# Optimization experiments

Hardware: AMD Instinct MI355X
Metric: run time of the kernel (lower is better)

The kernel has to match this reference:

```python
import jax, jax.numpy as jnp
import numpy as np

N = 32768          # total nodes
B = 64             # graphs
NPG = N // B       # nodes per graph (equal-sized graphs)
E = 524288         # edges (before self-loops)
D_IN, HID, HEADS, D_OUT = 128, 64, 4, 128
DH = HID * HEADS   # 256
NEG_SLOPE = 0.2
EPS = 1e-5

def _leaky(x):
    return jnp.where(x >= 0, x, NEG_SLOPE * x)

def gat_conv(x, src, dst, W, a_src, a_dst, b, concat):
    """PyG-style GATConv (self-loops already included in src/dst)."""
    H, C = a_src.shape
    h = (x @ W).reshape(N, H, C)                       # [N,H,C]
    es = jnp.einsum('nhc,hc->nh', h, a_src)            # score from source feats
    ed = jnp.einsum('nhc,hc->nh', h, a_dst)            # score from target feats
    e = _leaky(es[src] + ed[dst])                      # [E',H]
    m = jax.ops.segment_max(e, dst, num_segments=N)    # stable softmax per dst
    p = jnp.exp(e - m[dst])
    s = jax.ops.segment_sum(p, dst, num_segments=N)
    alpha = p / s[dst]                                 # [E',H]
    out = jax.ops.segment_sum(h[src] * alpha[..., None], dst, num_segments=N)
    out = out.reshape(N, H * C) if concat else out.mean(axis=1)
    return out + b

def mha(x, Wi, bi, Wo, bo, heads):
    """torch.nn.MultiheadAttention (batch_first, no mask, eval)."""
    Bb, T, D = x.shape
    qkv = x @ Wi.T + bi                                # [B,T,3D]
    q, k, v = jnp.split(qkv, 3, axis=-1)
    hd = D // heads
    def sp(t):
        return t.reshape(Bb, T, heads, hd).transpose(0, 2, 1, 3)  # [B,h,T,hd]
    q, k, v = sp(q), sp(k), sp(v)
    scores = jnp.einsum('bhqd,bhkd->bhqk', q, k) / jnp.sqrt(jnp.float32(hd))
    attn = jax.nn.softmax(scores, axis=-1)
    o = jnp.einsum('bhqk,bhkd->bhqd', attn, v)
    o = o.transpose(0, 2, 1, 3).reshape(Bb, T, D)
    return o @ Wo.T + bo

def layer_norm(x, g, b):
    mu = x.mean(-1, keepdims=True)
    var = x.var(-1, keepdims=True)
    return (x - mu) / jnp.sqrt(var + EPS) * g + b

def setup_inputs() -> dict:
    key = jax.random.key(0)
    ks = jax.random.split(key, 20)
    s = 0.1
    inp = {
        'x': jax.random.normal(ks[0], (N, D_IN), jnp.float32),
        'edge_index': jax.random.randint(ks[1], (2, E), 0, N, jnp.int64),
        'batch': (jnp.arange(N, dtype=jnp.int64) // NPG),
        # gat1: D_IN -> HEADS*HID (concat)
        'W1': jax.random.normal(ks[2], (D_IN, HEADS * HID), jnp.float32) * s,
        'aS1': jax.random.normal(ks[3], (HEADS, HID), jnp.float32) * s,
        'aD1': jax.random.normal(ks[4], (HEADS, HID), jnp.float32) * s,
        'b1': jnp.zeros((HEADS * HID,), jnp.float32),
        # gat2: DH -> HEADS*HID (concat)
        'W2': jax.random.normal(ks[5], (DH, HEADS * HID), jnp.float32) * s,
        'aS2': jax.random.normal(ks[6], (HEADS, HID), jnp.float32) * s,
        'aD2': jax.random.normal(ks[7], (HEADS, HID), jnp.float32) * s,
        'b2': jnp.zeros((HEADS * HID,), jnp.float32),
        # gat3: DH -> D_OUT, heads=1, concat=False (mean)
        'W3': jax.random.normal(ks[8], (DH, D_OUT), jnp.float32) * s,
        'aS3': jax.random.normal(ks[9], (1, D_OUT), jnp.float32) * s,
        'aD3': jax.random.normal(ks[10], (1, D_OUT), jnp.float32) * s,
        'b3': jnp.zeros((D_OUT,), jnp.float32),
        # MultiheadAttention
        'Wi': jax.random.normal(ks[11], (3 * DH, DH), jnp.float32) * s,
        'bi': jnp.zeros((3 * DH,), jnp.float32),
        'Wo': jax.random.normal(ks[12], (DH, DH), jnp.float32) * s,
        'bo': jnp.zeros((DH,), jnp.float32),
        # LayerNorm
        'gamma': jnp.ones((DH,), jnp.float32),
        'beta': jnp.zeros((DH,), jnp.float32),
    }
    return inp

def reference(x, edge_index, batch, W1, aS1, aD1, b1, W2, aS2, aD2, b2,
              W3, aS3, aD3, b3, Wi, bi, Wo, bo, gamma, beta):
    # add self-loops (PyG GATConv default)
    loops = jnp.arange(N, dtype=edge_index.dtype)
    src = jnp.concatenate([edge_index[0], loops])
    dst = jnp.concatenate([edge_index[1], loops])

    x1 = jax.nn.elu(gat_conv(x, src, dst, W1, aS1, aD1, b1, concat=True))
    x2 = jax.nn.elu(gat_conv(x1, src, dst, W2, aS2, aD2, b2, concat=True))

    # ragged-to-dense batching: batch = arange(N)//NPG (equal-sized, sorted),
    # so the torch python loop reduces to a reshape with no padding.
    x2b = x2.reshape(B, NPG, DH)
    attended = mha(x2b, Wi, bi, Wo, bo, HEADS).reshape(N, DH)

    x2a = layer_norm(attended + x2, gamma, beta)
    x3 = gat_conv(x2a, src, dst, W3, aS3, aD3, b3, concat=False)
    return x3
```

## Files before the change

kernel.cpp:

```cpp
#include <hip/hip_runtime.h>

typedef _Float16 half_t;
typedef _Float16 half8  __attribute__((ext_vector_type(8)));
typedef _Float16 half4v __attribute__((ext_vector_type(4)));
typedef float    f32x4  __attribute__((ext_vector_type(4)));

constexpr int N_NODES = 32768;
constexpr int NPG_    = 512;

#define MFMA16(a, b, c) __builtin_amdgcn_mfma_f32_16x16x32_f16((a), (b), (c), 0, 0, 0)

__device__ __forceinline__ void gload_lds16(const half_t* g, half_t* l) {
  __builtin_amdgcn_global_load_lds(
      (const __attribute__((address_space(1))) void*)g,
      (__attribute__((address_space(3))) void*)l, 16, 0, 0);
}

__global__ void k_hist(const int* __restrict__ dst, int* __restrict__ deg, int E) {
  int i = blockIdx.x * 256 + threadIdx.x;
  if (i < E) atomicAdd(&deg[dst[i]], 1);
}

__global__ __launch_bounds__(1024) void k_scan(const int* __restrict__ deg,
                                               int* __restrict__ rowptr) {
  __shared__ int part[1024];
  int t = threadIdx.x;
  int base = t * 32;
  int s = 0;
  #pragma unroll
  for (int i = 0; i < 32; i++) s += deg[base + i];
  part[t] = s;
  __syncthreads();
  for (int off = 1; off < 1024; off <<= 1) {
    int add = (t >= off) ? part[t - off] : 0;
    __syncthreads();
    part[t] += add;
    __syncthreads();
  }
  int run = (t == 0) ? 0 : part[t - 1];
  for (int i = 0; i < 32; i++) { rowptr[base + i] = run; run += deg[base + i]; }
  if (t == 1023) rowptr[N_NODES] = run;
}

__global__ void k_selfloop(const int* __restrict__ rowptr, int* __restrict__ fill,
                           int* __restrict__ col) {
  int i = blockIdx.x * 256 + threadIdx.x;
  fill[i] = 1;
  col[rowptr[i]] = i;
}

__global__ void k_scatter(const int* __restrict__ src, const int* __restrict__ dst,
                          const int* __restrict__ rowptr, int* __restrict__ fill,
                          int* __restrict__ col, int E) {
  int i = blockIdx.x * 256 + threadIdx.x;
  if (i < E) {
    int d = dst[i];
    int pos = rowptr[d] + atomicAdd(&fill[d], 1);
    col[pos] = src[i];
  }
}

__global__ void k_convert(
    const float* __restrict__ x,  half_t* __restrict__ x_h,
    const float* __restrict__ W1, half_t* __restrict__ W1t,
    const float* __restrict__ W2, half_t* __restrict__ W2t,
    const float* __restrict__ W3, half_t* __restrict__ W3t,
    const float* __restrict__ Wi, half_t* __restrict__ Wi_h,
    const float* __restrict__ Wo, half_t* __restrict__ Wo_h,
    int* __restrict__ deg)
{
  int bid = blockIdx.x, t = threadIdx.x;
  if (bid < 16384) {
    int i = bid * 256 + t;
    x_h[i] = (half_t)x[i];
  } else if (bid < 16512) {
    int i = (bid - 16384) * 256 + t;
    int o = i >> 7, k = i & 127;
    W1t[i] = (half_t)W1[k * 256 + o];
  } else if (bid < 16768) {
    int i = (bid - 16512) * 256 + t;
    int o = i >> 8, k = i & 255;
    W2t[i] = (half_t)W2[k * 256 + o];
  } else if (bid < 16896) {
    int i = (bid - 16768) * 256 + t;
    int o = i >> 8, k = i & 255;
    W3t[i] = (half_t)W3[k * 128 + o];
  } else if (bid < 17664) {
    int i = (bid - 16896) * 256 + t;
    Wi_h[i] = (half_t)Wi[i];
  } else if (bid < 17920) {
    int i = (bid - 17664) * 256 + t;
    Wo_h[i] = (half_t)Wo[i];
  } else {
    deg[(bid - 17920) * 256 + t] = 1;
  }
}

__global__ __launch_bounds__(256) void k_gemm(
    const half_t* __restrict__ A, const half_t* __restrict__ Bt,
    const float* __restrict__ bias, int bias_per_row,
    half_t* __restrict__ outh, float* __restrict__ outf,
    int M, int Nc, int K,
    const float* __restrict__ aS, const float* __restrict__ aD,
    float* __restrict__ es, float* __restrict__ ed, int H)
{
  __shared__ __align__(16) half_t As[128 * 64];
  __shared__ __align__(16) half_t Bs[128 * 64];
  __shared__ float sRed[2][4][64];
  int w = threadIdx.x >> 6, lane = threadIdx.x & 63;
  int r = lane & 15, q = lane >> 4;
  int m0 = blockIdx.y * 128, n0 = blockIdx.x * 128;
  int mh = (w & 1) * 64, nh = (w >> 1) * 64;
  f32x4 acc[4][4];
  #pragma unroll
  for (int i = 0; i < 4; i++)
    #pragma unroll
    for (int j = 0; j < 4; j++) acc[i][j] = f32x4{0.f, 0.f, 0.f, 0.f};

  int srow = lane >> 3;
  int sc   = lane & 7;

  for (int k0 = 0; k0 < K; k0 += 64) {
    __syncthreads();
    #pragma unroll
    for (int i = 0; i < 4; i++) {
      int R0 = w * 32 + i * 8;
      int row = R0 + srow;
      int cg = sc ^ (row & 7);
      gload_lds16(A  + (size_t)(m0 + row) * K + k0 + cg * 8, &As[R0 * 64]);
      gload_lds16(Bt + (size_t)(n0 + row) * K + k0 + cg * 8, &Bs[R0 * 64]);
    }
    __syncthreads();
    #pragma unroll
    for (int kk = 0; kk < 2; kk++) {
      half8 af[4], bf[4];
      #pragma unroll
      for (int t = 0; t < 4; t++) {
        int rr = mh + t * 16 + r;
        af[t] = *(const half8*)&As[rr * 64 + (((kk * 4 + q) ^ (rr & 7)) << 3)];
      }
      #pragma unroll
      for (int t = 0; t < 4; t++) {
        int rr = nh + t * 16 + r;
        bf[t] = *(const half8*)&Bs[rr * 64 + (((kk * 4 + q) ^ (rr & 7)) << 3)];
      }
      #pragma unroll
      for (int ti = 0; ti < 4; ti++)
        #pragma unroll
        for (int tj = 0; tj < 4; tj++)
          acc[ti][tj] = MFMA16(af[ti], bf[tj], acc[ti][tj]);
    }
  }

  #pragma unroll
  for (int tj = 0; tj < 4; tj++) {
    int colc = n0 + nh + tj * 16 + r;
    #pragma unroll
    for (int ti = 0; ti < 4; ti++) {
      #pragma unroll
      for (int i = 0; i < 4; i++) {
        int row = m0 + mh + ti * 16 + q * 4 + i;
        float bv = bias ? (bias_per_row ? bias[row] : bias[colc]) : 0.f;
        float v = acc[ti][tj][i] + bv;
        size_t idx = (size_t)row * Nc + colc;
        if (outf) outf[idx] = v;
        if (outh) outh[idx] = (half_t)v;
      }
    }
  }

  if (es) {
    if (H == 4) {
      int head = (n0 >> 6) + (nh >> 6);
      float aSv[4], aDv[4];
      #pragma unroll
      for (int tj = 0; tj < 4; tj++) {
        int cl = tj * 16 + r;
        aSv[tj] = aS[head * 64 + cl];
        aDv[tj] = aD[head * 64 + cl];
      }
      #pragma unroll
      for (int ti = 0; ti < 4; ti++) {
        #pragma unroll
        for (int i = 0; i < 4; i++) {
          float ps = 0.f, pd = 0.f;
          #pragma unroll
          for (int tj = 0; tj < 4; tj++) {
            float av = acc[ti][tj][i];
            ps += av * aSv[tj];
            pd += av * aDv[tj];
          }
          #pragma unroll
          for (int off = 1; off < 16; off <<= 1) {
            ps += __shfl_xor(ps, off);
            pd += __shfl_xor(pd, off);
          }
          if (r == 0) {
            int row = m0 + mh + ti * 16 + q * 4 + i;
            es[(size_t)row * 4 + head] = ps;
            ed[(size_t)row * 4 + head] = pd;
          }
        }
      }
    } else {
      float aSv[4], aDv[4];
      #pragma unroll
      for (int tj = 0; tj < 4; tj++) {
        int c = nh + tj * 16 + r;
        aSv[tj] = aS[c];
        aDv[tj] = aD[c];
      }
      #pragma unroll
      for (int ti = 0; ti < 4; ti++) {
        #pragma unroll
        for (int i = 0; i < 4; i++) {
          float ps = 0.f, pd = 0.f;
          #pragma unroll
          for (int tj = 0; tj < 4; tj++) {
            float av = acc[ti][tj][i];
            ps += av * aSv[tj];
            pd += av * aDv[tj];
          }
          #pragma unroll
          for (int off = 1; off < 16; off <<= 1) {
            ps += __shfl_xor(ps, off);
            pd += __shfl_xor(pd, off);
          }
          if (r == 0) {
            int ri = ti * 16 + q * 4 + i;
            sRed[0][w][ri] = ps;
            sRed[1][w][ri] = pd;
          }
        }
      }
      __syncthreads();
      if (threadIdx.x < 128) {
        int row = threadIdx.x;
        int wlo = row >> 6, ri = row & 63;
        es[m0 + row] = sRed[0][wlo][ri] + sRed[0][wlo + 2][ri];
        ed[m0 + row] = sRed[1][wlo][ri] + sRed[1][wlo + 2][ri];
      }
    }
  }
}

__global__ __launch_bounds__(256) void k_gemm_ln(
    const half_t* __restrict__ A, const half_t* __restrict__ Bt,
    const float* __restrict__ bias, const half_t* __restrict__ res,
    const float* __restrict__ gamma, const float* __restrict__ beta,
    half_t* __restrict__ outh)
{
  __shared__ __align__(16) half_t As[64 * 64];
  __shared__ __align__(16) half_t Bs[256 * 64];
  __shared__ float sSum[4][64], sSq[4][64];
  __shared__ float sMR[64][2];
  int w = threadIdx.x >> 6, lane = threadIdx.x & 63;
  int r = lane & 15, q = lane >> 4;
  int m0 = blockIdx.x * 64;
  int nh = w * 64;
  f32x4 acc[4][4];
  #pragma unroll
  for (int i = 0; i < 4; i++)
    #pragma unroll
    for (int j = 0; j < 4; j++) acc[i][j] = f32x4{0.f, 0.f, 0.f, 0.f};

  int srow = lane >> 3, sc = lane & 7;

  for (int k0 = 0; k0 < 256; k0 += 64) {
    __syncthreads();
    #pragma unroll
    for (int i = 0; i < 2; i++) {
      int R0 = w * 16 + i * 8;
      int row = R0 + srow;
      int cg = sc ^ (row & 7);
      gload_lds16(A + (size_t)(m0 + row) * 256 + k0 + cg * 8, &As[R0 * 64]);
    }
    #pragma unroll
    for (int i = 0; i < 8; i++) {
      int R0 = w * 64 + i * 8;
      int row = R0 + srow;
      int cg = sc ^ (row & 7);
      gload_lds16(Bt + (size_t)row * 256 + k0 + cg * 8, &Bs[R0 * 64]);
    }
    __syncthreads();
    #pragma unroll
    for (int kk = 0; kk < 2; kk++) {
      half8 af[4], bf[4];
      #pragma unroll
      for (int t = 0; t < 4; t++) {
        int rr = t * 16 + r;
        af[t] = *(const half8*)&As[rr * 64 + (((kk * 4 + q) ^ (rr & 7)) << 3)];
      }
      #pragma unroll
      for (int t = 0; t < 4; t++) {
        int rr = nh + t * 16 + r;
        bf[t] = *(const half8*)&Bs[rr * 64 + (((kk * 4 + q) ^ (rr & 7)) << 3)];
      }
      #pragma unroll
      for (int ti = 0; ti < 4; ti++)
        #pragma unroll
        for (int tj = 0; tj < 4; tj++)
          acc[ti][tj] = MFMA16(af[ti], bf[tj], acc[ti][tj]);
    }
  }

  float gv[4], bv[4];
  #pragma unroll
  for (int tj = 0; tj < 4; tj++) {
    int col = nh + tj * 16 + r;
    gv[tj] = gamma[col];
    bv[tj] = beta[col];
  }
  #pragma unroll
  for (int ti = 0; ti < 4; ti++) {
    #pragma unroll
    for (int i = 0; i < 4; i++) {
      int row = ti * 16 + q * 4 + i;
      float s = 0.f, ss = 0.f;
      #pragma unroll
      for (int tj = 0; tj < 4; tj++) {
        int col = nh + tj * 16 + r;
        float v = acc[ti][tj][i] + bias[col]
                + (float)res[(size_t)(m0 + row) * 256 + col];
        acc[ti][tj][i] = v;
        s += v;
        ss += v * v;
      }
      #pragma unroll
      for (int off = 1; off < 16; off <<= 1) {
        s  += __shfl_xor(s, off);
        ss += __shfl_xor(ss, off);
      }
      if (r == 0) { sSum[w][row] = s; sSq[w][row] = ss; }
    }
  }
  __syncthreads();
  if (threadIdx.x < 64) {
    int row = threadIdx.x;
    float s  = sSum[0][row] + sSum[1][row] + sSum[2][row] + sSum[3][row];
    float ss = sSq[0][row] + sSq[1][row] + sSq[2][row] + sSq[3][row];
    float mean = s * (1.f / 256.f);
    float var  = ss * (1.f / 256.f) - mean * mean;
    sMR[row][0] = mean;
    sMR[row][1] = rsqrtf(var + 1e-5f);
  }
  __syncthreads();
  #pragma unroll
  for (int ti = 0; ti < 4; ti++) {
    #pragma unroll
    for (int i = 0; i < 4; i++) {
      int row = ti * 16 + q * 4 + i;
      float mean = sMR[row][0], rstd = sMR[row][1];
      #pragma unroll
      for (int tj = 0; tj < 4; tj++) {
        int col = nh + tj * 16 + r;
        outh[(size_t)(m0 + row) * 256 + col] =
            (half_t)((acc[ti][tj][i] - mean) * rstd * gv[tj] + bv[tj]);
      }
    }
  }
}

template<int HC, int H, bool FP16ACC>
__global__ __launch_bounds__(256) void k_agg(
    const half_t* __restrict__ h, const float* __restrict__ es,
    const float* __restrict__ ed, const float* __restrict__ bias,
    const int* __restrict__ rowptr, const int* __restrict__ col, int elu,
    float* __restrict__ outf, half_t* __restrict__ outh)
{
  constexpr int VPT = HC / 16;
  constexpr int NV8 = VPT / 8;
  constexpr int C = HC / H;
  int lane = threadIdx.x & 63;
  int g = lane >> 4, li = lane & 15;
  int n = blockIdx.x * 4 + (threadIdx.x >> 6);
  int cbase = li * VPT;
  int hl = cbase / C;
  float edn = ed[(size_t)n * H + hl];
  int j0 = rowptr[n], j1 = rowptr[n + 1];
  const half_t* hb = h + cbase;

  float sum0 = 0.f, sum1 = 0.f;

  if constexpr (FP16ACC) {
    half8 acc0[NV8], acc1[NV8];
    #pragma unroll
    for (int i = 0; i < NV8; i++) {
      acc0[i] = half8{0, 0, 0, 0, 0, 0, 0, 0};
      acc1[i] = half8{0, 0, 0, 0, 0, 0, 0, 0};
    }
    for (int j = j0 + g; j < j1; j += 8) {
      int jb = j + 4;
      int s0 = col[j];
      int s1 = col[(jb < j1) ? jb : j];
      float e0 = es[(size_t)s0 * H + hl] + edn;
      e0 = fmaxf(e0, 0.2f * e0);
      float e1 = es[(size_t)s1 * H + hl] + edn;
      e1 = fmaxf(e1, 0.2f * e1);
      e1 = (jb < j1) ? e1 : -1e30f;
      const half_t* hp0 = hb + (size_t)s0 * HC;
      const half_t* hp1 = hb + (size_t)s1 * HC;
      float p0 = exp2f(e0 * 1.44269504f - 8.65617025f);
      float p1 = exp2f(e1 * 1.44269504f - 8.65617025f);
      sum0 += p0; sum1 += p1;
      half_t q0 = (half_t)p0, q1 = (half_t)p1;
      half8 pv0 = {q0, q0, q0, q0, q0, q0, q0, q0};
      half8 pv1 = {q1, q1, q1, q1, q1, q1, q1, q1};
      #pragma unroll
      for (int i = 0; i < NV8; i++) {
        half8 v0 = *(const half8*)(hp0 + i * 8);
        half8 v1 = *(const half8*)(hp1 + i * 8);
        acc0[i] += pv0 * v0;
        acc1[i] += pv1 * v1;
      }
    }
    float sum = sum0 + sum1;
    sum += __shfl_xor(sum, 16);
    sum += __shfl_xor(sum, 32);
    float av[VPT];
    #pragma unroll
    for (int i = 0; i < VPT; i++) {
      av[i] = (float)acc0[i >> 3][i & 7] + (float)acc1[i >> 3][i & 7];
      av[i] += __shfl_xor(av[i], 16);
      av[i] += __shfl_xor(av[i], 32);
    }
    float inv = 1.f / sum;
    float v[VPT];
    #pragma unroll
    for (int i = 0; i < VPT; i++) {
      float t = av[i] * inv + bias[cbase + i];
      if (elu) t = (t > 0.f) ? t : __expf(t) - 1.f;
      v[i] = t;
    }
    if (g == 0) {
      size_t obase = (size_t)n * HC + cbase;
      if (outh) {
        #pragma unroll
        for (int p8 = 0; p8 < NV8; p8++) {
          half8 hv;
          #pragma unroll
          for (int i = 0; i < 8; i++) hv[i] = (half_t)v[p8 * 8 + i];
          *(half8*)(outh + obase + p8 * 8) = hv;
        }
      }
      if (outf) {
        #pragma unroll
        for (int p4 = 0; p4 < VPT / 4; p4++) {
          float4 fv = {v[p4 * 4], v[p4 * 4 + 1], v[p4 * 4 + 2], v[p4 * 4 + 3]};
          *(float4*)(outf + obase + p4 * 4) = fv;
        }
      }
    }
  } else {
    float acc0[VPT], acc1[VPT];
    #pragma unroll
    for (int i = 0; i < VPT; i++) { acc0[i] = 0.f; acc1[i] = 0.f; }
    for (int j = j0 + g; j < j1; j += 8) {
      int jb = j + 4;
      int s0 = col[j];
      int s1 = col[(jb < j1) ? jb : j];
      float e0 = es[(size_t)s0 * H + hl] + edn;
      e0 = fmaxf(e0, 0.2f * e0);
      float e1 = es[(size_t)s1 * H + hl] + edn;
      e1 = fmaxf(e1, 0.2f * e1);
      e1 = (jb < j1) ? e1 : -1e30f;
      const half_t* hp0 = hb + (size_t)s0 * HC;
      const half_t* hp1 = hb + (size_t)s1 * HC;
      float p0 = __expf(e0), p1 = __expf(e1);
      sum0 += p0; sum1 += p1;
      #pragma unroll
      for (int c8 = 0; c8 < NV8; c8++) {
        half8 a0 = *(const half8*)(hp0 + c8 * 8);
        half8 a1 = *(const half8*)(hp1 + c8 * 8);
        #pragma unroll
        for (int i = 0; i < 8; i++) {
          acc0[c8 * 8 + i] += p0 * (float)a0[i];
          acc1[c8 * 8 + i] += p1 * (float)a1[i];
        }
      }
    }
    float sum = sum0 + sum1;
    sum += __shfl_xor(sum, 16);
    sum += __shfl_xor(sum, 32);
    float av[VPT];
    #pragma unroll
    for (int i = 0; i < VPT; i++) {
      av[i] = acc0[i] + acc1[i];
      av[i] += __shfl_xor(av[i], 16);
      av[i] += __shfl_xor(av[i], 32);
    }
    float inv = 1.f / sum;
    float v[VPT];
    #pragma unroll
    for (int i = 0; i < VPT; i++) {
      float t = av[i] * inv + bias[cbase + i];
      if (elu) t = (t > 0.f) ? t : __expf(t) - 1.f;
      v[i] = t;
    }
    if (g == 0) {
      size_t obase = (size_t)n * HC + cbase;
      if (outh) {
        #pragma unroll
        for (int p8 = 0; p8 < NV8; p8++) {
          half8 hv;
          #pragma unroll
          for (int i = 0; i < 8; i++) hv[i] = (half_t)v[p8 * 8 + i];
          *(half8*)(outh + obase + p8 * 8) = hv;
        }
      }
      if (outf) {
        #pragma unroll
        for (int p4 = 0; p4 < VPT / 4; p4++) {
          float4 fv = {v[p4 * 4], v[p4 * 4 + 1], v[p4 * 4 + 2], v[p4 * 4 + 3]};
          *(float4*)(outf + obase + p4 * 4) = fv;
        }
      }
    }
  }
}

__global__ __launch_bounds__(256) void k_attn(
    const half_t* __restrict__ qk, const half_t* __restrict__ vt,
    half_t* __restrict__ o)
{
  __shared__ __align__(16) half_t Kt[64 * 64];
  __shared__ __align__(16) half_t Vt[64 * 64];
  __shared__ __align__(16) half_t Pb[4][16][72];

  int pair = blockIdx.x;
  int b = pair >> 2, hh = pair & 3;
  int q0 = blockIdx.y * 64;
  int w = threadIdx.x >> 6, lane = threadIdx.x & 63;
  int cc = lane & 15, qq = lane >> 4;

  const half_t* Qp = qk + ((size_t)(b * NPG_ + q0 + w * 16 + cc) * 512 + hh * 64);
  half8 qa0 = *(const half8*)(Qp + qq * 8);
  half8 qa1 = *(const half8*)(Qp + 32 + qq * 8);

  f32x4 oacc[4];
  #pragma unroll
  for (int t = 0; t < 4; t++) oacc[t] = f32x4{0.f, 0.f, 0.f, 0.f};
  float rs = 0.f;

  const half_t* kb = qk + ((size_t)(b * NPG_) * 512 + 256 + hh * 64);
  const half_t* vb = vt + ((size_t)(hh * 64) * 32768 + b * NPG_);

  int krow = lane >> 3, ksl = lane & 7;

  for (int kt = 0; kt < 8; kt++) {
    __syncthreads();
    #pragma unroll
    for (int i = 0; i < 2; i++) {
      int R = w * 16 + i * 8;
      int kr = R + krow;
      gload_lds16(kb + (size_t)(kt * 64 + kr) * 512 + ((ksl ^ (kr & 7)) * 8),
                  &Kt[R * 64]);
      gload_lds16(vb + (size_t)kr * 32768 + kt * 64 + ((ksl ^ (kr & 7)) * 8),
                  &Vt[R * 64]);
    }
    __syncthreads();

    #pragma unroll
    for (int mt = 0; mt < 4; mt++) {
      int key = mt * 16 + cc;
      half8 k0 = *(const half8*)&Kt[key * 64 + ((qq ^ (key & 7)) << 3)];
      half8 k1 = *(const half8*)&Kt[key * 64 + (((qq + 4) ^ (key & 7)) << 3)];
      f32x4 s = f32x4{0.f, 0.f, 0.f, 0.f};
      s = MFMA16(k0, qa0, s);
      s = MFMA16(k1, qa1, s);
      half4v ph;
      #pragma unroll
      for (int i = 0; i < 4; i++) {
        float p = exp2f(s[i] * 0.180336886f - 11.54156033f);
        rs += p;
        ph[i] = (half_t)p;
      }
      *(half4v*)&Pb[w][cc][mt * 16 + qq * 4] = ph;
    }

    #pragma unroll
    for (int kc = 0; kc < 2; kc++) {
      half8 a = *(const half8*)&Pb[w][cc][kc * 32 + qq * 8];
      #pragma unroll
      for (int nt = 0; nt < 4; nt++) {
        int d = nt * 16 + cc;
        half8 bb = *(const half8*)&Vt[d * 64 + (((kc * 4 + qq) ^ (d & 7)) << 3)];
        oacc[nt] = MFMA16(a, bb, oacc[nt]);
      }
    }
  }

  rs += __shfl_xor(rs, 16);
  rs += __shfl_xor(rs, 32);
  #pragma unroll
  for (int i = 0; i < 4; i++) {
    float rsv = __shfl(rs, qq * 4 + i);
    float inv = 1.f / rsv;
    int node = b * NPG_ + q0 + w * 16 + qq * 4 + i;
    #pragma unroll
    for (int nt = 0; nt < 4; nt++)
      o[(size_t)node * 256 + hh * 64 + nt * 16 + cc] = (half_t)(oacc[nt][i] * inv);
  }
}

extern "C" void kernel_launch(void* const* d_in, const int* in_sizes, int n_in,
                              void* d_out, int out_size, void* d_ws, size_t ws_size,
                              hipStream_t stream)
{
  const float* x    = (const float*)d_in[0];
  const int*   ei   = (const int*)d_in[1];
  const float* W1   = (const float*)d_in[3];
  const float* aS1  = (const float*)d_in[4];
  const float* aD1  = (const float*)d_in[5];
  const float* b1   = (const float*)d_in[6];
  const float* W2   = (const float*)d_in[7];
  const float* aS2  = (const float*)d_in[8];
  const float* aD2  = (const float*)d_in[9];
  const float* b2   = (const float*)d_in[10];
  const float* W3   = (const float*)d_in[11];
  const float* aS3  = (const float*)d_in[12];
  const float* aD3  = (const float*)d_in[13];
  const float* b3   = (const float*)d_in[14];
  const float* Wi   = (const float*)d_in[15];
  const float* bi   = (const float*)d_in[16];
  const float* Wo   = (const float*)d_in[17];
  const float* bo   = (const float*)d_in[18];
  const float* gam  = (const float*)d_in[19];
  const float* bet  = (const float*)d_in[20];
  float* out = (float*)d_out;
  const int N = N_NODES;
  int E = in_sizes[1] / 2;

  char* ws = (char*)d_ws;
  size_t off = 0;
  auto alloc = [&](size_t bytes) -> void* {
    void* p = ws + off;
    off = (off + bytes + 255) & ~(size_t)255;
    return p;
  };
  half_t* x_h    = (half_t*)alloc((size_t)N * 128 * 2);
  half_t* h_h    = (half_t*)alloc((size_t)N * 256 * 2);
  half_t* x1_h   = (half_t*)alloc((size_t)N * 256 * 2);
  half_t* x2_h   = (half_t*)alloc((size_t)N * 256 * 2);
  half_t* qk_h   = (half_t*)alloc((size_t)N * 512 * 2);
  half_t* vt_h   = (half_t*)alloc((size_t)256 * N * 2);
  half_t* o_h    = (half_t*)alloc((size_t)N * 256 * 2);
  half_t* x2a_h  = (half_t*)alloc((size_t)N * 256 * 2);
  half_t* W1t    = (half_t*)alloc(256 * 128 * 2);
  half_t* W2t    = (half_t*)alloc(256 * 256 * 2);
  half_t* W3t    = (half_t*)alloc(128 * 256 * 2);
  half_t* Wi_h   = (half_t*)alloc(768 * 256 * 2);
  half_t* Wo_h   = (half_t*)alloc(256 * 256 * 2);
  float*  es     = (float*) alloc((size_t)N * 4 * 4);
  float*  ed     = (float*) alloc((size_t)N * 4 * 4);
  int*    deg    = (int*)   alloc((size_t)N * 4);
  int*    fill   = (int*)   alloc((size_t)N * 4);
  int*    rowptr = (int*)   alloc(((size_t)N + 1) * 4);
  int*    col    = (int*)   alloc((size_t)(N + E) * 4);

  const int* srcE = ei;
  const int* dstE = ei + E;

  k_convert<<<18048, 256, 0, stream>>>(x, x_h, W1, W1t, W2, W2t, W3, W3t,
                                       Wi, Wi_h, Wo, Wo_h, deg);
  k_hist<<<(E + 255) / 256, 256, 0, stream>>>(dstE, deg, E);
  k_scan<<<1, 1024, 0, stream>>>(deg, rowptr);
  k_selfloop<<<N / 256, 256, 0, stream>>>(rowptr, fill, col);
  k_scatter<<<(E + 255) / 256, 256, 0, stream>>>(srcE, dstE, rowptr, fill, col, E);

  k_gemm<<<dim3(2, N / 128), 256, 0, stream>>>(x_h, W1t, nullptr, 0, h_h, nullptr,
                                               N, 256, 128, aS1, aD1, es, ed, 4);
  k_agg<256, 4, true><<<N / 4, 256, 0, stream>>>(h_h, es, ed, b1, rowptr, col, 1, nullptr, x1_h);

  k_gemm<<<dim3(2, N / 128), 256, 0, stream>>>(x1_h, W2t, nullptr, 0, h_h, nullptr,
                                               N, 256, 256, aS2, aD2, es, ed, 4);
  k_agg<256, 4, true><<<N / 4, 256, 0, stream>>>(h_h, es, ed, b2, rowptr, col, 1, nullptr, x2_h);

  k_gemm<<<dim3(4, N / 128), 256, 0, stream>>>(x2_h, Wi_h, bi, 0, qk_h, nullptr,
                                               N, 512, 256, nullptr, nullptr, nullptr, nullptr, 0);
  k_gemm<<<dim3(N / 128, 2), 256, 0, stream>>>(Wi_h + 512 * 256, x2_h, bi + 512, 1,
                                               vt_h, nullptr, 256, N, 256,
                                               nullptr, nullptr, nullptr, nullptr, 0);
  k_attn<<<dim3(256, 8), 256, 0, stream>>>(qk_h, vt_h, o_h);

  k_gemm_ln<<<N / 64, 256, 0, stream>>>(o_h, Wo_h, bo, x2_h, gam, bet, x2a_h);

  k_gemm<<<dim3(1, N / 128), 256, 0, stream>>>(x2a_h, W3t, nullptr, 0, h_h, nullptr,
                                               N, 128, 256, aS3, aD3, es, ed, 1);
  k_agg<128, 1, false><<<N / 4, 256, 0, stream>>>(h_h, es, ed, b3, rowptr, col, 0, out, nullptr);
}
```

Baseline: 446.1 us.

## Replace single-block CSR scan with three-phase multi-block scan

Result: no change. 442.3 us (-0.8%).

```diff
diff --git a/kernel.cpp b/kernel.cpp
--- a/kernel.cpp
+++ b/kernel.cpp
@@ -21,32 +21,57 @@
   if (i < E) atomicAdd(&deg[dst[i]], 1);
 }
 
-__global__ __launch_bounds__(1024) void k_scan(const int* __restrict__ deg,
+__global__ __launch_bounds__(256) void k_scan1(const int* __restrict__ deg,
+                                               int* __restrict__ partial,
+                                               int* __restrict__ blockSums) {
+  __shared__ int sd[256];
+  int t = threadIdx.x;
+  int i = blockIdx.x * 256 + t;
+  int v = deg[i];
+  sd[t] = v;
+  __syncthreads();
+  int acc = v;
+  for (int off = 1; off < 256; off <<= 1) {
+    int add = (t >= off) ? sd[t - off] : 0;
+    __syncthreads();
+    acc += add;
+    sd[t] = acc;
+    __syncthreads();
+  }
+  partial[i] = acc - v;
+  if (t == 255) blockSums[blockIdx.x] = acc;
+}
+
+__global__ __launch_bounds__(128) void k_scan2(const int* __restrict__ blockSums,
+                                               int* __restrict__ blockOff,
                                                int* __restrict__ rowptr) {
-  __shared__ int part[1024];
+  __shared__ int sd[128];
   int t = threadIdx.x;
-  int base = t * 32;
-  int s = 0;
-  #pragma unroll
-  for (int i = 0; i < 32; i++) s += deg[base + i];
-  part[t] = s;
+  int v = blockSums[t];
+  sd[t] = v;
   __syncthreads();
-  for (int off = 1; off < 1024; off <<= 1) {
-    int add = (t >= off) ? part[t - off] : 0;
-    __syncthreads();
-    part[t] += add;
-    __syncthreads();
-  }
-  int run = (t == 0) ? 0 : part[t - 1];
-  for (int i = 0; i < 32; i++) { rowptr[base + i] = run; run += deg[base + i]; }
-  if (t == 1023) rowptr[N_NODES] = run;
-}
-
-__global__ void k_selfloop(const int* __restrict__ rowptr, int* __restrict__ fill,
-                           int* __restrict__ col) {
+  int acc = v;
+  for (int off = 1; off < 128; off <<= 1) {
+    int add = (t >= off) ? sd[t - off] : 0;
+    __syncthreads();
+    acc += add;
+    sd[t] = acc;
+    __syncthreads();
+  }
+  blockOff[t] = acc - v;
+  if (t == 127) rowptr[N_NODES] = acc;
+}
+
+__global__ __launch_bounds__(256) void k_scan3(const int* __restrict__ partial,
+                                               const int* __restrict__ blockOff,
+                                               int* __restrict__ rowptr,
+                                               int* __restrict__ fill,
+                                               int* __restrict__ col) {
   int i = blockIdx.x * 256 + threadIdx.x;
+  int rp = partial[i] + blockOff[blockIdx.x];
+  rowptr[i] = rp;
   fill[i] = 1;
-  col[rowptr[i]] = i;
+  col[rp] = i;
 }
 
 __global__ void k_scatter(const int* __restrict__ src, const int* __restrict__ dst,
@@ -657,6 +682,9 @@
   int*    fill   = (int*)   alloc((size_t)N * 4);
   int*    rowptr = (int*)   alloc(((size_t)N + 1) * 4);
   int*    col    = (int*)   alloc((size_t)(N + E) * 4);
+  int*    part   = (int*)   alloc((size_t)N * 4);
+  int*    bsum   = (int*)   alloc(128 * 4);
+  int*    boff   = (int*)   alloc(128 * 4);
 
   const int* srcE = ei;
   const int* dstE = ei + E;
@@ -664,8 +692,9 @@
   k_convert<<<18048, 256, 0, stream>>>(x, x_h, W1, W1t, W2, W2t, W3, W3t,
                                        Wi, Wi_h, Wo, Wo_h, deg);
   k_hist<<<(E + 255) / 256, 256, 0, stream>>>(dstE, deg, E);
-  k_scan<<<1, 1024, 0, stream>>>(deg, rowptr);
-  k_selfloop<<<N / 256, 256, 0, stream>>>(rowptr, fill, col);
+  k_scan1<<<128, 256, 0, stream>>>(deg, part, bsum);
+  k_scan2<<<1, 128, 0, stream>>>(bsum, boff, rowptr);
+  k_scan3<<<128, 256, 0, stream>>>(part, boff, rowptr, fill, col);
   k_scatter<<<(E + 255) / 256, 256, 0, stream>>>(srcE, dstE, rowptr, fill, col, E);
 
   k_gemm<<<dim3(2, N / 128), 256, 0, stream>>>(x_h, W1t, nullptr, 0, h_h, nullptr,
```
